# Performance work log

Hardware: AMD Instinct MI355X
Metric: run time of the kernel (lower is better)

The kernel has to match this reference:

```python
import jax, jax.numpy as jnp
import numpy as np

KERNEL_MUL = 2.0
KERNEL_NUM = 5
EPS = 1e-8


def setup_inputs() -> dict:
    key = jax.random.key(0)
    k1, k2 = jax.random.split(key)
    source = jax.random.normal(k1, (4096, 512), dtype=jnp.float32)
    target = jax.random.normal(k2, (4096, 512), dtype=jnp.float32)
    return {"source": source, "target": target}


def reference(source, target):
    ns = source.shape[0]
    total = jnp.concatenate([source, target], axis=0)          # (N, D)
    n = total.shape[0]
    # Pairwise squared L2 via the matmul identity ||a-b||^2 = ||a||^2 + ||b||^2 - 2 a.b
    sq = jnp.sum(total * total, axis=1)                        # (N,)
    gram = total @ total.T                                     # (N, N)
    l2 = jnp.maximum(sq[:, None] + sq[None, :] - 2.0 * gram, 0.0)
    # Adaptive bandwidth: mean of off-diagonal distances (diagonal is 0)
    bandwidth = jnp.sum(l2) / (n * n - n)
    # Multi-bandwidth RBF kernel sum
    half = KERNEL_NUM // 2
    kernel = jnp.zeros_like(l2)
    for i in range(KERNEL_NUM):
        bw = bandwidth * (KERNEL_MUL ** (i - half))
        kernel = kernel + jnp.exp(-l2 / (bw + EPS))
    xx = jnp.mean(kernel[:ns, :ns])
    yy = jnp.mean(kernel[ns:, ns:])
    xy = jnp.mean(kernel[:ns, ns:])
    return xx + yy - 2.0 * xy
```

## Files before the change

kernel.cpp:

```cpp
#include <hip/hip_runtime.h>
#include <stdint.h>

typedef uint8_t u8;
typedef uint16_t u16;
typedef uint32_t u32;
typedef unsigned long long u64;

#define NS 4096
#define NTOT 8192
#define DIM 512
#define NTILE 2080
#define GRID_MMD 1024

typedef __attribute__((ext_vector_type(2))) long l64x2;
typedef __attribute__((ext_vector_type(4))) float f32x4;

__device__ inline void load_lds16(const void* g, void* l) {
    __builtin_amdgcn_global_load_lds((__attribute__((address_space(1))) void*)g,
                                     (__attribute__((address_space(3))) void*)l,
                                     16, 0, 0);
}


__global__ __launch_bounds__(256) void k_prep(const float* __restrict__ src,
                                              const float* __restrict__ tgt,
                                              u8* __restrict__ Tb,
                                              float* __restrict__ sq,
                                              float* __restrict__ cp) {
    __shared__ u8 xb[2][16][528];
    __shared__ float cs_l[4][DIM];
    const int b = blockIdx.x, tid = threadIdx.x;
    const int w = tid >> 6, lane = tid & 63;
    const int rbl = w >> 1;
    const int i0 = (w & 1) * 8;

    float cs[8];
#pragma unroll
    for (int e = 0; e < 8; ++e) cs[e] = 0.f;

#pragma unroll
    for (int i = 0; i < 8; ++i) {
        const int fr = i0 + i;
        const int r = b * 32 + rbl * 16 + fr;
        const float* rowp = (r < NS) ? (src + (size_t)r * DIM)
                                     : (tgt + (size_t)(r - NS) * DIM);
        float4 v0 = *(const float4*)(rowp + lane * 8);
        float4 v1 = *(const float4*)(rowp + lane * 8 + 4);
        float vx[8] = {v0.x, v0.y, v0.z, v0.w, v1.x, v1.y, v1.z, v1.w};
        float ss = 0.f;
#pragma unroll
        for (int e = 0; e < 8; ++e) { ss += vx[e] * vx[e]; cs[e] += vx[e]; }
        int dlo = 0, dhi = 0;
        dlo = __builtin_amdgcn_cvt_pk_fp8_f32(vx[0], vx[1], dlo, 0);
        dlo = __builtin_amdgcn_cvt_pk_fp8_f32(vx[2], vx[3], dlo, 1);
        dhi = __builtin_amdgcn_cvt_pk_fp8_f32(vx[4], vx[5], dhi, 0);
        dhi = __builtin_amdgcn_cvt_pk_fp8_f32(vx[6], vx[7], dhi, 1);
        *(u32*)&xb[rbl][fr][lane * 8] = (u32)dlo;
        *(u32*)&xb[rbl][fr][lane * 8 + 4] = (u32)dhi;
#pragma unroll
        for (int off = 32; off; off >>= 1) ss += __shfl_down(ss, off);
        if (lane == 0) sq[r] = ss;
    }
#pragma unroll
    for (int e = 0; e < 8; ++e) cs_l[w][lane * 8 + e] = cs[e];
    __syncthreads();

    const int row = lane & 15, oct = lane >> 4;
#pragma unroll
    for (int ff = 0; ff < 4; ++ff) {
        const int f = w * 4 + ff;
        const int frbl = f >> 3, kt2 = f & 7;
        u64 a0 = *(const u64*)&xb[frbl][row][kt2 * 64 + oct * 8];
        u64 a1 = *(const u64*)&xb[frbl][row][kt2 * 64 + 32 + oct * 8];
        const int rbg = b * 2 + frbl;
        u8* dst = Tb + (size_t)(rbg * 8 + kt2) * 1024 + lane * 16;
        *(u64*)dst = a0;
        *(u64*)(dst + 8) = a1;
    }

    float a0 = cs_l[0][tid] + cs_l[1][tid] + cs_l[2][tid] + cs_l[3][tid];
    float a1 = cs_l[0][tid + 256] + cs_l[1][tid + 256] + cs_l[2][tid + 256] + cs_l[3][tid + 256];
    cp[(size_t)b * DIM + tid] = a0;
    cp[(size_t)b * DIM + tid + 256] = a1;
}

__global__ __launch_bounds__(256) void k_band(const float* __restrict__ sq,
                                              const float* __restrict__ cp,
                                              float* __restrict__ scales,
                                              double* __restrict__ accum,
                                              u32* __restrict__ counter) {
    __shared__ double red[4];
    const int tid = threadIdx.x;
    const int w = tid >> 6, lane = tid & 63;

    double ssq = 0.0;
    for (int i = tid; i < NTOT; i += 256) ssq += (double)sq[i];

    double s2 = 0.0;
#pragma unroll
    for (int cc = 0; cc < 2; ++cc) {
        const int c = tid + cc * 256;
        float b0 = 0.f, b1 = 0.f, b2 = 0.f, b3 = 0.f;
#pragma unroll 8
        for (int k = 0; k < 256; k += 4) {
            b0 += cp[(size_t)(k + 0) * DIM + c];
            b1 += cp[(size_t)(k + 1) * DIM + c];
            b2 += cp[(size_t)(k + 2) * DIM + c];
            b3 += cp[(size_t)(k + 3) * DIM + c];
        }
        double sc = (double)b0 + (double)b1 + (double)b2 + (double)b3;
        s2 += sc * sc;
    }

    auto blkreduce = [&](double v) -> double {
#pragma unroll
        for (int off = 32; off; off >>= 1) v += __shfl_down(v, off);
        __syncthreads();
        if (lane == 0) red[w] = v;
        __syncthreads();
        return red[0] + red[1] + red[2] + red[3];
    };
    double sumsq = blkreduce(ssq);
    double s2t = blkreduce(s2);

    if (tid < 5) {
        const double nn = (double)NTOT;
        double bw = (2.0 * nn * sumsq - 2.0 * s2t) / (nn * nn - nn);
        const double fac[5] = {0.25, 0.5, 1.0, 2.0, 4.0};
        scales[tid] = (float)(-1.0 / (bw * fac[tid] + 1e-8));
    }
    if (tid == 5) *accum = 0.0;
    if (tid == 6) *counter = 0u;
}

__global__ __launch_bounds__(256) void k_mmd(const u8* __restrict__ Tb,
                                             const float* __restrict__ sq,
                                             const float* __restrict__ scales,
                                             double* __restrict__ accum,
                                             u32* __restrict__ counter,
                                             float* __restrict__ out) {
    __shared__ __align__(16) u8 As[3][8192];
    __shared__ __align__(16) u8 Bs[3][8192];
    __shared__ double red[4];

    const int tid = threadIdx.x;
    const int wid = tid >> 6, lane = tid & 63;
    const int wr = wid >> 1, wc = wid & 1;
    const int fr = lane & 15, fq = lane >> 4;
    const float s2c = scales[2];

    const int b = (int)blockIdx.x;
    const int bp = (b & 7) * (GRID_MMD / 8) + (b >> 3);
    const int lo = (bp * 65) >> 5;
    const int hi = ((bp + 1) * 65) >> 5;

    double lacc_tot = 0.0;

    for (int t = lo; t < hi; ++t) {
        int bi = (int)((sqrtf(8.0f * (float)t + 1.0f) - 1.0f) * 0.5f);
        while ((bi + 1) * (bi + 2) / 2 <= t) ++bi;
        while (bi * (bi + 1) / 2 > t) --bi;
        const int bj = t - bi * (bi + 1) / 2;

        u32 offA[2], offB[2];
#pragma unroll
        for (int q = 0; q < 2; ++q) {
            offA[q] = (u32)((bi * 8 + wid * 2 + q) * 8) * 1024 + lane * 16;
            offB[q] = (u32)((bj * 8 + wid * 2 + q) * 8) * 1024 + lane * 16;
        }

        auto stage = [&](int buf, int u) {
#pragma unroll
            for (int q = 0; q < 2; ++q) {
                load_lds16(Tb + offA[q] + u * 1024, &As[buf][(wid * 2 + q) * 1024]);
                load_lds16(Tb + offB[q] + u * 1024, &Bs[buf][(wid * 2 + q) * 1024]);
            }
        };

        f32x4 acc[4][4];
#pragma unroll
        for (int m = 0; m < 4; ++m)
#pragma unroll
            for (int n = 0; n < 4; ++n) acc[m][n] = (f32x4){0.f, 0.f, 0.f, 0.f};

        __builtin_amdgcn_s_barrier();
        asm volatile("" ::: "memory");

        stage(0, 0);
        stage(1, 1);

#pragma unroll
        for (int u = 0; u < 8; ++u) {
            if (u == 7) asm volatile("s_waitcnt vmcnt(0)" ::: "memory");
            else        asm volatile("s_waitcnt vmcnt(4)" ::: "memory");
            __builtin_amdgcn_s_barrier();
            asm volatile("" ::: "memory");

            const u8* Ab = As[u % 3];
            const u8* Bb = Bs[u % 3];
            l64x2 av[4], bv[4];
#pragma unroll
            for (int m = 0; m < 4; ++m)
                av[m] = *(const l64x2*)(Ab + (wr * 4 + m) * 1024 + lane * 16);
#pragma unroll
            for (int n = 0; n < 4; ++n)
                bv[n] = *(const l64x2*)(Bb + (wc * 4 + n) * 1024 + lane * 16);
#pragma unroll
            for (int m = 0; m < 4; ++m)
#pragma unroll
                for (int n = 0; n < 4; ++n) {
                    acc[m][n] = __builtin_amdgcn_mfma_f32_16x16x32_fp8_fp8(
                        av[m].x, bv[n].x, acc[m][n], 0, 0, 0);
                    acc[m][n] = __builtin_amdgcn_mfma_f32_16x16x32_fp8_fp8(
                        av[m].y, bv[n].y, acc[m][n], 0, 0, 0);
                }

            if (u + 2 < 8) stage((u + 2) % 3, u + 2);
        }

        const int rowA0 = bi * 128, rowB0 = bj * 128;
        float sqc[4];
#pragma unroll
        for (int n = 0; n < 4; ++n) sqc[n] = sq[rowB0 + wc * 64 + n * 16 + fr];

        float facc = 0.f;
#pragma unroll
        for (int m = 0; m < 4; ++m) {
            float4 s4 = *(const float4*)(sq + rowA0 + wr * 64 + m * 16 + fq * 4);
            float sqr[4] = {s4.x, s4.y, s4.z, s4.w};
#pragma unroll
            for (int n = 0; n < 4; ++n) {
#pragma unroll
                for (int r = 0; r < 4; ++r) {
                    float g = acc[m][n][r];
                    float l2 = fmaxf(sqr[r] + sqc[n] - 2.0f * g, 0.0f);
                    float e = __expf(s2c * l2);
                    float e2 = e * e;
                    float e4 = e2 * e2;
                    float r1, r2;
                    asm("v_sqrt_f32 %0, %1" : "=v"(r1) : "v"(e));
                    asm("v_sqrt_f32 %0, %1" : "=v"(r2) : "v"(r1));
                    facc += e4 + e2 + e + r1 + r2;
                }
            }
        }

        const double wfac = ((bi == bj) ? 1.0 : 2.0) *
                            (((bi < 32) == (bj < 32)) ? 1.0 : -1.0);
        lacc_tot += (double)facc * wfac;
    }

    double v = lacc_tot;
#pragma unroll
    for (int off = 32; off; off >>= 1) v += __shfl_down(v, off);
    __syncthreads();
    if (lane == 0) red[wid] = v;
    __syncthreads();

    if (tid == 0) {
        atomicAdd(accum, red[0] + red[1] + red[2] + red[3]);
        __threadfence();
        u32 done = atomicAdd(counter, 1u);
        if (done == GRID_MMD - 1) {
            double tot = atomicAdd(accum, 0.0);
            out[0] = (float)(tot / ((double)NS * (double)NS));
        }
    }
}

extern "C" void kernel_launch(void* const* d_in, const int* in_sizes, int n_in,
                              void* d_out, int out_size, void* d_ws, size_t ws_size,
                              hipStream_t stream) {
    const float* src = (const float*)d_in[0];
    const float* tgt = (const float*)d_in[1];
    char* ws = (char*)d_ws;

    const size_t MB4 = 4u * 1024 * 1024;
    u8* Tb        = (u8*)ws;
    float* sq     = (float*)(ws + MB4);
    float* cp     = (float*)(ws + MB4 + 32 * 1024);
    float* scales = (float*)(ws + MB4 + 544 * 1024);
    double* accum = (double*)(ws + MB4 + 544 * 1024 + 128);
    u32* counter  = (u32*)(ws + MB4 + 544 * 1024 + 192);

    k_prep<<<256, 256, 0, stream>>>(src, tgt, Tb, sq, cp);
    k_band<<<1, 256, 0, stream>>>(sq, cp, scales, accum, counter);
    k_mmd<<<GRID_MMD, 256, 0, stream>>>(Tb, sq, scales, accum, counter, (float*)d_out);
}
```

Baseline: 146.0 us.

## Prefetch next tile's first K-chunks during epilogue and shrink MMD grid

The fp8 MFMA MMD kernel now walks its triangular tile range incrementally instead of recomputing the tile index with a sqrt each iteration. It issues the next tile's first two K-slice loads into LDS while the current tile's exp/sqrt epilogue runs, which hides the pipeline fill latency at each tile boundary. The grid drops from 1024 to 768 blocks, with a general division-based split of the 2080 tiles, so three blocks fit per CU in a single wave. The cost is a redundant prefetch on each block's last tile and a coarser tile split, some blocks doing 2 tiles and others 3.

```diff
diff --git a/kernel.cpp b/kernel.cpp
--- a/kernel.cpp
+++ b/kernel.cpp
@@ -10,7 +10,7 @@
 #define NTOT 8192
 #define DIM 512
 #define NTILE 2080
-#define GRID_MMD 1024
+#define GRID_MMD 768
 
 typedef __attribute__((ext_vector_type(2))) long l64x2;
 typedef __attribute__((ext_vector_type(4))) float f32x4;
@@ -151,43 +151,42 @@
 
     const int b = (int)blockIdx.x;
     const int bp = (b & 7) * (GRID_MMD / 8) + (b >> 3);
-    const int lo = (bp * 65) >> 5;
-    const int hi = ((bp + 1) * 65) >> 5;
+    const int lo = (int)(((long)bp * NTILE) / GRID_MMD);
+    const int hi = (int)(((long)(bp + 1) * NTILE) / GRID_MMD);
+
+    int bi = (int)((sqrtf(8.0f * (float)lo + 1.0f) - 1.0f) * 0.5f);
+    while ((bi + 1) * (bi + 2) / 2 <= lo) ++bi;
+    while (bi * (bi + 1) / 2 > lo) --bi;
+    int bj = lo - bi * (bi + 1) / 2;
+
+    auto stageAB = [&](int tbi, int tbj, int buf, int u) {
+#pragma unroll
+        for (int q = 0; q < 2; ++q) {
+            const int c = wid * 2 + q;
+            load_lds16(Tb + (((tbi * 8 + c) * 8 + u) << 10) + lane * 16,
+                       &As[buf][c * 1024]);
+            load_lds16(Tb + (((tbj * 8 + c) * 8 + u) << 10) + lane * 16,
+                       &Bs[buf][c * 1024]);
+        }
+    };
 
     double lacc_tot = 0.0;
 
+    stageAB(bi, bj, 0, 0);
+    stageAB(bi, bj, 1, 1);
+
     for (int t = lo; t < hi; ++t) {
-        int bi = (int)((sqrtf(8.0f * (float)t + 1.0f) - 1.0f) * 0.5f);
-        while ((bi + 1) * (bi + 2) / 2 <= t) ++bi;
-        while (bi * (bi + 1) / 2 > t) --bi;
-        const int bj = t - bi * (bi + 1) / 2;
-
-        u32 offA[2], offB[2];
-#pragma unroll
-        for (int q = 0; q < 2; ++q) {
-            offA[q] = (u32)((bi * 8 + wid * 2 + q) * 8) * 1024 + lane * 16;
-            offB[q] = (u32)((bj * 8 + wid * 2 + q) * 8) * 1024 + lane * 16;
-        }
-
-        auto stage = [&](int buf, int u) {
-#pragma unroll
-            for (int q = 0; q < 2; ++q) {
-                load_lds16(Tb + offA[q] + u * 1024, &As[buf][(wid * 2 + q) * 1024]);
-                load_lds16(Tb + offB[q] + u * 1024, &Bs[buf][(wid * 2 + q) * 1024]);
-            }
-        };
+        int nbi = bi, nbj = bj;
+        if (t + 1 < hi) {
+            nbj = bj + 1;
+            if (nbj > nbi) { nbi = bi + 1; nbj = 0; }
+        }
 
         f32x4 acc[4][4];
 #pragma unroll
         for (int m = 0; m < 4; ++m)
 #pragma unroll
             for (int n = 0; n < 4; ++n) acc[m][n] = (f32x4){0.f, 0.f, 0.f, 0.f};
-
-        __builtin_amdgcn_s_barrier();
-        asm volatile("" ::: "memory");
-
-        stage(0, 0);
-        stage(1, 1);
 
 #pragma unroll
         for (int u = 0; u < 8; ++u) {
@@ -215,8 +214,13 @@
                         av[m].y, bv[n].y, acc[m][n], 0, 0, 0);
                 }
 
-            if (u + 2 < 8) stage((u + 2) % 3, u + 2);
-        }
+            if (u + 2 < 8) stageAB(bi, bj, (u + 2) % 3, u + 2);
+            if (u == 7) stageAB(nbi, nbj, 0, 0);
+        }
+
+        __builtin_amdgcn_s_barrier();
+        asm volatile("" ::: "memory");
+        stageAB(nbi, nbj, 1, 1);
 
         const int rowA0 = bi * 128, rowB0 = bj * 128;
         float sqc[4];
@@ -248,6 +252,8 @@
         const double wfac = ((bi == bj) ? 1.0 : 2.0) *
                             (((bi < 32) == (bj < 32)) ? 1.0 : -1.0);
         lacc_tot += (double)facc * wfac;
+
+        bi = nbi; bj = nbj;
     }
 
     double v = lacc_tot;
```

Measured after the change: 136.7 us. -6.4%, faster.
